# Kernel tuning notes

Hardware: AMD Instinct MI355X
Metric: run time of the kernel (lower is better)

Reference implementation:

```python
import jax, jax.numpy as jnp
import numpy as np

B, S, IK, IV = 16, 2048, 3, 1
D = IK + IV          # input_size = 4
H = 256              # hidden_size
F = 512              # dim_feedforward
L = 2                # num_layers
EPS = 1e-5


def setup_inputs() -> dict:
    key = jax.random.key(0)
    ks = jax.random.split(key, 16)
    n = jax.random.normal
    inp = {
        'KEY': n(ks[0], (B, S, IK), jnp.float32),
        'VALUE': n(ks[1], (B, S, IV), jnp.float32),
        # per-layer kernel-attention projections (stacked on layer axis)
        'Wq': n(ks[2], (L, D, H), jnp.float32) * 0.1,
        'bq': jnp.zeros((L, H), jnp.float32),
        'Wk': n(ks[3], (L, D, H), jnp.float32) * 0.1,
        'bk': jnp.zeros((L, H), jnp.float32),
        'Wv': n(ks[4], (L, D, H), jnp.float32) * 0.1,
        'bv': jnp.zeros((L, H), jnp.float32),
        'Wo': n(ks[5], (L, H, D), jnp.float32) * 0.1,
        'bo': jnp.zeros((L, D), jnp.float32),
        'bw': jnp.ones((L,), jnp.float32),          # Gaussian kernel bandwidth
        # LayerNorm 1
        'g1': jnp.ones((L, D), jnp.float32),
        'be1': jnp.zeros((L, D), jnp.float32),
        # FFN
        'W1': n(ks[6], (L, D, F), jnp.float32) * 0.1,
        'b1': jnp.zeros((L, F), jnp.float32),
        'W2': n(ks[7], (L, F, D), jnp.float32) * 0.1,
        'b2': jnp.zeros((L, D), jnp.float32),
        # LayerNorm 2
        'g2': jnp.ones((L, D), jnp.float32),
        'be2': jnp.zeros((L, D), jnp.float32),
        # final fc: input_size -> input_v
        'Wfc': n(ks[8], (D, IV), jnp.float32) * 0.1,
        'bfc': jnp.zeros((IV,), jnp.float32),
    }
    return inp


def _layernorm(x, g, b):
    m = x.mean(-1, keepdims=True)
    v = ((x - m) ** 2).mean(-1, keepdims=True)
    return (x - m) * jax.lax.rsqrt(v + EPS) * g + b


def reference(KEY, VALUE, Wq, bq, Wk, bk, Wv, bv, Wo, bo, bw,
              g1, be1, W1, b1, W2, b2, g2, be2, Wfc, bfc):
    # positioning: concat coords and values -> [B, S, D]
    X = jnp.concatenate([KEY, VALUE], axis=-1)
    n_layers = Wq.shape[0]
    for i in range(n_layers):
        # Nadaraya-Watson Gaussian kernel attention (madsnn, type='nwd', kernel='gauss')
        Q = X @ Wq[i] + bq[i]                      # [B,S,H]
        K = X @ Wk[i] + bk[i]                      # [B,S,H]
        V = X @ Wv[i] + bv[i]                      # [B,S,H]
        # pairwise squared distances ||q-k||^2, [B,S,S]
        d2 = ((Q * Q).sum(-1)[:, :, None]
              + (K * K).sum(-1)[:, None, :]
              - 2.0 * jnp.einsum('bqh,bkh->bqk', Q, K))
        attn = jax.nn.softmax(-0.5 * d2 * (bw[i] ** 2), axis=-1)
        attn_out = jnp.einsum('bqk,bkh->bqh', attn, V) @ Wo[i] + bo[i]  # [B,S,D]
        # residual + LayerNorm + FFN + residual + LayerNorm (dropout = identity in eval)
        res = _layernorm(X + attn_out, g1[i], be1[i])
        ff = jax.nn.relu(res @ W1[i] + b1[i]) @ W2[i] + b2[i]
        X = _layernorm(res + ff, g2[i], be2[i])
    return X @ Wfc + bfc                            # [B,S,IV]
```

## Files before the change

### kernel.cpp

```cpp
#include <hip/hip_runtime.h>

#define BB 16
#define SS 2048
#define NTOK (BB*SS)
#define NPAIR (NTOK/2)
#define PLANE (NPAIR*4)
#define FF 512
#define EPSF 1e-5f

#if __has_builtin(__builtin_amdgcn_exp2f)
#define EXP2F(x) __builtin_amdgcn_exp2f(x)
#else
#define EXP2F(x) exp2f(x)
#endif

typedef float v2f __attribute__((ext_vector_type(2)));


__device__ __forceinline__ float wred64(float v) {
#pragma unroll
  for (int m = 32; m > 0; m >>= 1) v += __shfl_xor(v, m, 64);
  return v;
}

__device__ __forceinline__ float rflf(float v) {
  union { float f; int i; } u; u.f = v;
  u.i = __builtin_amdgcn_readfirstlane(u.i);
  return u.f;
}


__global__ __launch_bounds__(64) void prep_kernel(
    const float* __restrict__ Wq, const float* __restrict__ bq,
    const float* __restrict__ Wk, const float* __restrict__ bk,
    const float* __restrict__ Wv, const float* __restrict__ bv,
    const float* __restrict__ Wo, const float* __restrict__ bw,
    const float* __restrict__ W1, const float* __restrict__ b1,
    const float* __restrict__ W2,
    float* __restrict__ sm, float* __restrict__ w1t)
{
  const int i = blockIdx.x;
  const int lane = threadIdx.x;
  float m4[4][4] = {{0}}, gkk[4][4] = {{0}}, wvo[4][4] = {{0}};
  float akk[4] = {0}, bvo[4] = {0};
  float ck1 = 0.f, ck2 = 0.f;

  for (int h = lane; h < 256; h += 64) {
    float vq[4], vk[4], vv[4], wo4[4];
#pragma unroll
    for (int a = 0; a < 4; ++a) {
      vq[a]  = Wq[(i*4 + a)*256 + h];
      vk[a]  = Wk[(i*4 + a)*256 + h];
      vv[a]  = Wv[(i*4 + a)*256 + h];
      wo4[a] = Wo[(i*256 + h)*4 + a];
    }
    const float bqh = bq[i*256 + h], bkh = bk[i*256 + h], bvh = bv[i*256 + h];
#pragma unroll
    for (int a = 0; a < 4; ++a) {
#pragma unroll
      for (int c = 0; c < 4; ++c) {
        m4[a][c]  = fmaf(vq[a], vk[c], m4[a][c]);
        gkk[a][c] = fmaf(vk[a], vk[c], gkk[a][c]);
        wvo[a][c] = fmaf(vv[a], wo4[c], wvo[a][c]);
      }
      akk[a] = fmaf(vk[a], bqh - bkh, akk[a]);
      bvo[a] = fmaf(bvh, wo4[a], bvo[a]);
    }
    ck1 = fmaf(bqh, bkh, ck1);
    ck2 = fmaf(bkh, bkh, ck2);
  }
#pragma unroll
  for (int a = 0; a < 4; ++a) {
#pragma unroll
    for (int c = 0; c < 4; ++c) {
      m4[a][c]  = wred64(m4[a][c]);
      gkk[a][c] = wred64(gkk[a][c]);
      wvo[a][c] = wred64(wvo[a][c]);
    }
    akk[a] = wred64(akk[a]);
    bvo[a] = wred64(bvo[a]);
  }
  ck1 = wred64(ck1); ck2 = wred64(ck2);

  if (lane == 0) {
    const float bwv = bw[i];
    const float bw2 = bwv * bwv * 1.44269504088896f;
    float* s = sm + i*64;
#pragma unroll
    for (int a = 0; a < 4; ++a) {
#pragma unroll
      for (int c = 0; c < 4; ++c) {
        s[a*4+c]      = bw2 * m4[a][c];
        s[16 + a*4+c] = -0.5f * bw2 * gkk[a][c];
        s[32 + a*4+c] = wvo[a][c];
      }
      s[48+a] = bw2 * akk[a];
      s[52+a] = bvo[a];
    }
    s[56] = bw2 * (ck1 - 0.5f * ck2);
  }
  for (int f = lane; f < FF; f += 64) {
    float* rec = w1t + (i*FF + f)*12;
#pragma unroll
    for (int c = 0; c < 4; ++c) rec[c]   = W1[(i*4 + c)*FF + f];
#pragma unroll
    for (int c = 0; c < 4; ++c) rec[4+c] = W2[(i*FF + f)*4 + c];
    rec[8] = b1[i*FF + f];
    rec[9] = 0.f; rec[10] = 0.f; rec[11] = 0.f;
  }
}

__device__ __forceinline__ void compute_feat(const float x[4], const float* __restrict__ s,
                                             float* __restrict__ featrec)
{
  float P[4], VT[4], tk[4];
#pragma unroll
  for (int a = 0; a < 4; ++a) {
    P[a]  = fmaf(s[a*4+3], x[3], fmaf(s[a*4+2], x[2], fmaf(s[a*4+1], x[1], s[a*4+0]*x[0])));
    tk[a] = fmaf(s[16+a*4+3], x[3], fmaf(s[16+a*4+2], x[2], fmaf(s[16+a*4+1], x[1], s[16+a*4+0]*x[0])));
    VT[a] = s[52+a] + fmaf(s[32+3*4+a], x[3], fmaf(s[32+2*4+a], x[2], fmaf(s[32+1*4+a], x[1], s[32+0*4+a]*x[0])));
  }
  float R = s[56];
#pragma unroll
  for (int a = 0; a < 4; ++a) R = fmaf(tk[a] + s[48+a], x[a], R);
  featrec[0]=P[0]; featrec[1]=P[1]; featrec[2]=P[2]; featrec[3]=P[3];
  featrec[4]=VT[0]; featrec[5]=VT[1]; featrec[6]=VT[2]; featrec[7]=VT[3];
  featrec[8]=R;
}

__global__ __launch_bounds__(256) void feat_kernel(
    const float* __restrict__ KEY, const float* __restrict__ VALUE,
    const float* __restrict__ sm, float* __restrict__ feat)
{
  const int p = blockIdx.x*256 + threadIdx.x;
  const int ta = 2*p, tb = 2*p + 1;
  float xa[4] = {KEY[ta*3], KEY[ta*3+1], KEY[ta*3+2], VALUE[ta]};
  float xb[4] = {KEY[tb*3], KEY[tb*3+1], KEY[tb*3+2], VALUE[tb]};
  float fa[9], fb[9];
  compute_feat(xa, sm, fa);
  compute_feat(xb, sm, fb);
#pragma unroll
  for (int pl = 0; pl < 4; ++pl) {
    *(float4*)(feat + (size_t)pl*PLANE + (size_t)p*4) =
        make_float4(fa[2*pl], fb[2*pl], fa[2*pl+1], fb[2*pl+1]);
  }
  *(float4*)(feat + (size_t)4*PLANE + (size_t)p*4) =
      make_float4(fa[8], fb[8], 0.f, 0.f);
}

__device__ __forceinline__ void ln4(const float t[4], const float* __restrict__ g,
                                    const float* __restrict__ b, float r[4])
{
  const float m = 0.25f*(t[0]+t[1]+t[2]+t[3]);
  const float d0 = t[0]-m, d1 = t[1]-m, d2 = t[2]-m, d3 = t[3]-m;
  const float v = 0.25f*(d0*d0 + d1*d1 + d2*d2 + d3*d3);
  const float sc = rsqrtf(v + EPSF);
  r[0] = fmaf(d0*sc, g[0], b[0]);
  r[1] = fmaf(d1*sc, g[1], b[1]);
  r[2] = fmaf(d2*sc, g[2], b[2]);
  r[3] = fmaf(d3*sc, g[3], b[3]);
}

__global__ __launch_bounds__(512, 4) void layer_kernel(
    const float* __restrict__ KEY, const float* __restrict__ VALUE,
    const float* __restrict__ X, const float* __restrict__ feat,
    const float* __restrict__ w1t, const float* __restrict__ smn,
    const float* __restrict__ bo, const float* __restrict__ g1, const float* __restrict__ be1,
    const float* __restrict__ b2v, const float* __restrict__ g2, const float* __restrict__ be2,
    float* __restrict__ Xout, float* __restrict__ featout,
    const float* __restrict__ Wfc, const float* __restrict__ bfc,
    float* __restrict__ outp, int first, int last)
{
  const int bid = blockIdx.x;
  const int b = bid >> 5, qg = bid & 31;
  const int qbase = (b << 11) + (qg << 6);
  const int tid = threadIdx.x;
  const int lane = tid & 63, wv = tid >> 6;
  const int q0 = qbase + wv*8;

  __shared__ float sums[8*8*9];
  __shared__ float ress[64*4];
  __shared__ float redf[8*64*4];

  float qx0[8], qx1[8], qx2[8], qx3[8];
#pragma unroll
  for (int q = 0; q < 8; ++q) {
    const int gq = q0 + q;
    float a, bq_, c, d;
    if (first) {
      a = KEY[gq*3]; bq_ = KEY[gq*3+1]; c = KEY[gq*3+2]; d = VALUE[gq];
    } else {
      const float4 xv = *(const float4*)(X + (size_t)gq*4);
      a = xv.x; bq_ = xv.y; c = xv.z; d = xv.w;
    }
    qx0[q] = rflf(a); qx1[q] = rflf(bq_); qx2[q] = rflf(c); qx3[q] = rflf(d);
  }

  v2f aV0[8], aV1[8], aV2[8], aV3[8], aD[8];
#pragma unroll
  for (int q = 0; q < 8; ++q) {
    aV0[q] = v2f{0.f,0.f}; aV1[q] = v2f{0.f,0.f};
    aV2[q] = v2f{0.f,0.f}; aV3[q] = v2f{0.f,0.f};
    aD[q]  = v2f{0.f,0.f};
  }

  const int pb = (b << 10) + lane;
#pragma unroll 2
  for (int it = 0; it < 16; ++it) {
    const size_t p4 = (size_t)(pb + (it << 6)) * 4;
    const float4 A = *(const float4*)(feat + p4);
    const float4 Bf = *(const float4*)(feat + (size_t)PLANE + p4);
    const float4 C = *(const float4*)(feat + (size_t)2*PLANE + p4);
    const float4 D = *(const float4*)(feat + (size_t)3*PLANE + p4);
    const float4 E = *(const float4*)(feat + (size_t)4*PLANE + p4);
    const v2f P0 = v2f{A.x, A.y},  P1 = v2f{A.z, A.w};
    const v2f P2 = v2f{Bf.x, Bf.y}, P3 = v2f{Bf.z, Bf.w};
    const v2f V0 = v2f{C.x, C.y},  V1 = v2f{C.z, C.w};
    const v2f V2 = v2f{D.x, D.y},  V3 = v2f{D.z, D.w};
    const v2f Rp = v2f{E.x, E.y};
#pragma unroll
    for (int q = 0; q < 8; ++q) {
      v2f l = __builtin_elementwise_fma(P0, v2f{qx0[q], qx0[q]}, Rp);
      l = __builtin_elementwise_fma(P1, v2f{qx1[q], qx1[q]}, l);
      l = __builtin_elementwise_fma(P2, v2f{qx2[q], qx2[q]}, l);
      l = __builtin_elementwise_fma(P3, v2f{qx3[q], qx3[q]}, l);
      const v2f e = v2f{EXP2F(l.x), EXP2F(l.y)};
      aV0[q] = __builtin_elementwise_fma(e, V0, aV0[q]);
      aV1[q] = __builtin_elementwise_fma(e, V1, aV1[q]);
      aV2[q] = __builtin_elementwise_fma(e, V2, aV2[q]);
      aV3[q] = __builtin_elementwise_fma(e, V3, aV3[q]);
      aD[q] += e;
    }
  }

  float s[8][5];
#pragma unroll
  for (int q = 0; q < 8; ++q) {
    s[q][0] = aV0[q].x + aV0[q].y;
    s[q][1] = aV1[q].x + aV1[q].y;
    s[q][2] = aV2[q].x + aV2[q].y;
    s[q][3] = aV3[q].x + aV3[q].y;
    s[q][4] = aD[q].x + aD[q].y;
  }
#pragma unroll
  for (int q = 0; q < 8; ++q)
#pragma unroll
    for (int c = 0; c < 5; ++c) s[q][c] = wred64(s[q][c]);

  if (lane == 0) {
    float* dst = sums + wv*72;
#pragma unroll
    for (int q = 0; q < 8; ++q) {
#pragma unroll
      for (int c = 0; c < 5; ++c) dst[q*9 + c] = s[q][c];
    }
  }
  __syncthreads();

  if (tid < 64) {
    const float* sv = sums + tid*9;
    const float inv = 1.0f / sv[4];
    const int gq = qbase + tid;
    float xv0, xv1, xv2, xv3;
    if (first) {
      xv0 = KEY[gq*3]; xv1 = KEY[gq*3+1]; xv2 = KEY[gq*3+2]; xv3 = VALUE[gq];
    } else {
      const float4 xv = *(const float4*)(X + (size_t)gq*4);
      xv0 = xv.x; xv1 = xv.y; xv2 = xv.z; xv3 = xv.w;
    }
    float t4[4];
    t4[0] = xv0 + fmaf(sv[0], inv, bo[0]);
    t4[1] = xv1 + fmaf(sv[1], inv, bo[1]);
    t4[2] = xv2 + fmaf(sv[2], inv, bo[2]);
    t4[3] = xv3 + fmaf(sv[3], inv, bo[3]);
    float r[4];
    ln4(t4, g1, be1, r);
    *(float4*)(ress + tid*4) = make_float4(r[0], r[1], r[2], r[3]);
  }
  __syncthreads();

  const int tok = lane, fc = wv;
  const float4 rv = *(const float4*)(ress + tok*4);
  float fa0 = 0.f, fa1 = 0.f, fa2 = 0.f, fa3 = 0.f;
  const float* wt = w1t + (size_t)fc*64*12;
#pragma unroll 4
  for (int f = 0; f < 64; ++f) {
    const float* rec = wt + f*12;
    const float4 w1r = *(const float4*)rec;
    const float4 w2r = *(const float4*)(rec + 4);
    const float b1f = rec[8];
    float h = fmaf(rv.w, w1r.w, fmaf(rv.z, w1r.z, fmaf(rv.y, w1r.y, fmaf(rv.x, w1r.x, b1f))));
    h = fmaxf(h, 0.f);
    fa0 = fmaf(h, w2r.x, fa0);
    fa1 = fmaf(h, w2r.y, fa1);
    fa2 = fmaf(h, w2r.z, fa2);
    fa3 = fmaf(h, w2r.w, fa3);
  }
  *(float4*)(redf + (size_t)((fc << 6) + tok)*4) = make_float4(fa0, fa1, fa2, fa3);
  __syncthreads();

  if (tid < 64) {
    float t2[4];
#pragma unroll
    for (int c = 0; c < 4; ++c) {
      float sa = b2v[c];
#pragma unroll
      for (int k = 0; k < 8; ++k) sa += redf[(size_t)((k << 6) + tid)*4 + c];
      t2[c] = ress[tid*4 + c] + sa;
    }
    float y[4];
    ln4(t2, g2, be2, y);
    const int gq = qbase + tid;
    if (last) {
      outp[gq] = fmaf(y[3], Wfc[3], fmaf(y[2], Wfc[2], fmaf(y[1], Wfc[1], fmaf(y[0], Wfc[0], bfc[0]))));
    } else {
      *(float4*)(Xout + (size_t)gq*4) = make_float4(y[0], y[1], y[2], y[3]);
      float fr[9];
      compute_feat(y, smn, fr);
      const int p = gq >> 1, par = gq & 1;
#pragma unroll
      for (int c = 0; c < 8; ++c)
        featout[(size_t)(c >> 1)*PLANE + (size_t)p*4 + (c & 1)*2 + par] = fr[c];
      featout[(size_t)4*PLANE + (size_t)p*4 + par] = fr[8];
    }
  }
}

extern "C" void kernel_launch(void* const* d_in, const int* in_sizes, int n_in,
                              void* d_out, int out_size, void* d_ws, size_t ws_size,
                              hipStream_t stream)
{
  const float* KEY   = (const float*)d_in[0];
  const float* VALUE = (const float*)d_in[1];
  const float* Wq  = (const float*)d_in[2];
  const float* bq  = (const float*)d_in[3];
  const float* Wk  = (const float*)d_in[4];
  const float* bk  = (const float*)d_in[5];
  const float* Wv  = (const float*)d_in[6];
  const float* bv  = (const float*)d_in[7];
  const float* Wo  = (const float*)d_in[8];
  const float* bo  = (const float*)d_in[9];
  const float* bw  = (const float*)d_in[10];
  const float* g1  = (const float*)d_in[11];
  const float* be1 = (const float*)d_in[12];
  const float* W1  = (const float*)d_in[13];
  const float* b1  = (const float*)d_in[14];
  const float* W2  = (const float*)d_in[15];
  const float* b2  = (const float*)d_in[16];
  const float* g2  = (const float*)d_in[17];
  const float* be2 = (const float*)d_in[18];
  const float* Wfc = (const float*)d_in[19];
  const float* bfc = (const float*)d_in[20];
  float* out = (float*)d_out;

  float* w    = (float*)d_ws;
  float* sm   = w;
  float* w1t  = w + 128;
  float* X1   = w + 12416;
  float* f0   = w + 143488;
  float* f1   = w + 471168;

  prep_kernel<<<2, 64, 0, stream>>>(Wq, bq, Wk, bk, Wv, bv, Wo, bw,
                                    W1, b1, W2, sm, w1t);
  feat_kernel<<<64, 256, 0, stream>>>(KEY, VALUE, sm, f0);

  layer_kernel<<<512, 512, 0, stream>>>(KEY, VALUE, X1, f0,
      w1t, sm + 64,
      bo, g1, be1, b2, g2, be2,
      X1, f1, Wfc, bfc, out, 1, 0);

  layer_kernel<<<512, 512, 0, stream>>>(KEY, VALUE, X1, f1,
      w1t + FF*12, sm,
      bo + 4, g1 + 4, be1 + 4, b2 + 4, g2 + 4, be2 + 4,
      X1, f1, Wfc, bfc, out, 0, 1);
}
```

Measured before the change: 183.1 us.

## Double query work per wave and software-pipeline feature loads in layer kernel

Result: slower. 189.2 us (+3.4%).

```diff
diff --git a/kernel.cpp b/kernel.cpp
--- a/kernel.cpp
+++ b/kernel.cpp
@@ -7,6 +7,7 @@
 #define PLANE (NPAIR*4)
 #define FF 512
 #define EPSF 1e-5f
+#define QW 16
 
 #if __has_builtin(__builtin_amdgcn_exp2f)
 #define EXP2F(x) __builtin_amdgcn_exp2f(x)
@@ -161,7 +162,7 @@
   r[3] = fmaf(d3*sc, g[3], b[3]);
 }
 
-__global__ __launch_bounds__(512, 4) void layer_kernel(
+__global__ __launch_bounds__(256, 2) void layer_kernel(
     const float* __restrict__ KEY, const float* __restrict__ VALUE,
     const float* __restrict__ X, const float* __restrict__ feat,
     const float* __restrict__ w1t, const float* __restrict__ smn,
@@ -176,50 +177,45 @@
   const int qbase = (b << 11) + (qg << 6);
   const int tid = threadIdx.x;
   const int lane = tid & 63, wv = tid >> 6;
-  const int q0 = qbase + wv*8;
-
-  __shared__ float sums[8*8*9];
+  const int q0 = qbase + wv*QW;
+
+  __shared__ float sums[4*QW*9];
   __shared__ float ress[64*4];
-  __shared__ float redf[8*64*4];
-
-  float qx0[8], qx1[8], qx2[8], qx3[8];
-#pragma unroll
-  for (int q = 0; q < 8; ++q) {
+  __shared__ float redf[4*64*4];
+
+  float qx0[QW], qx1[QW], qx2[QW], qx3[QW];
+#pragma unroll
+  for (int q = 0; q < QW; ++q) {
     const int gq = q0 + q;
-    float a, bq_, c, d;
+    float a, b_, c, d;
     if (first) {
-      a = KEY[gq*3]; bq_ = KEY[gq*3+1]; c = KEY[gq*3+2]; d = VALUE[gq];
+      a = KEY[gq*3]; b_ = KEY[gq*3+1]; c = KEY[gq*3+2]; d = VALUE[gq];
     } else {
       const float4 xv = *(const float4*)(X + (size_t)gq*4);
-      a = xv.x; bq_ = xv.y; c = xv.z; d = xv.w;
-    }
-    qx0[q] = rflf(a); qx1[q] = rflf(bq_); qx2[q] = rflf(c); qx3[q] = rflf(d);
-  }
-
-  v2f aV0[8], aV1[8], aV2[8], aV3[8], aD[8];
-#pragma unroll
-  for (int q = 0; q < 8; ++q) {
+      a = xv.x; b_ = xv.y; c = xv.z; d = xv.w;
+    }
+    qx0[q] = rflf(a); qx1[q] = rflf(b_); qx2[q] = rflf(c); qx3[q] = rflf(d);
+  }
+
+  v2f aV0[QW], aV1[QW], aV2[QW], aV3[QW], aD[QW];
+#pragma unroll
+  for (int q = 0; q < QW; ++q) {
     aV0[q] = v2f{0.f,0.f}; aV1[q] = v2f{0.f,0.f};
     aV2[q] = v2f{0.f,0.f}; aV3[q] = v2f{0.f,0.f};
     aD[q]  = v2f{0.f,0.f};
   }
 
   const int pb = (b << 10) + lane;
-#pragma unroll 2
-  for (int it = 0; it < 16; ++it) {
-    const size_t p4 = (size_t)(pb + (it << 6)) * 4;
-    const float4 A = *(const float4*)(feat + p4);
-    const float4 Bf = *(const float4*)(feat + (size_t)PLANE + p4);
-    const float4 C = *(const float4*)(feat + (size_t)2*PLANE + p4);
-    const float4 D = *(const float4*)(feat + (size_t)3*PLANE + p4);
-    const float4 E = *(const float4*)(feat + (size_t)4*PLANE + p4);
-    const v2f P0 = v2f{A.x, A.y},  P1 = v2f{A.z, A.w};
+
+  auto PROC = [&](const float4& A, const float4& Bf, const float4& C,
+                  const float4& D, const float4& E) {
+    const v2f P0 = v2f{A.x, A.y},   P1 = v2f{A.z, A.w};
     const v2f P2 = v2f{Bf.x, Bf.y}, P3 = v2f{Bf.z, Bf.w};
-    const v2f V0 = v2f{C.x, C.y},  V1 = v2f{C.z, C.w};
-    const v2f V2 = v2f{D.x, D.y},  V3 = v2f{D.z, D.w};
+    const v2f V0 = v2f{C.x, C.y},   V1 = v2f{C.z, C.w};
+    const v2f V2 = v2f{D.x, D.y},   V3 = v2f{D.z, D.w};
     const v2f Rp = v2f{E.x, E.y};
 #pragma unroll
-    for (int q = 0; q < 8; ++q) {
+    for (int q = 0; q < QW; ++q) {
       v2f l = __builtin_elementwise_fma(P0, v2f{qx0[q], qx0[q]}, Rp);
       l = __builtin_elementwise_fma(P1, v2f{qx1[q], qx1[q]}, l);
       l = __builtin_elementwise_fma(P2, v2f{qx2[q], qx2[q]}, l);
@@ -231,11 +227,31 @@
       aV3[q] = __builtin_elementwise_fma(e, V3, aV3[q]);
       aD[q] += e;
     }
-  }
-
-  float s[8][5];
-#pragma unroll
-  for (int q = 0; q < 8; ++q) {
+  };
+
+#define LDCH(A_, B_, C_, D_, E_, it_) {                                  \
+    const size_t o = (size_t)(pb + ((it_) << 6)) * 4;                    \
+    A_ = *(const float4*)(feat + o);                                     \
+    B_ = *(const float4*)(feat + (size_t)PLANE + o);                     \
+    C_ = *(const float4*)(feat + (size_t)2*PLANE + o);                   \
+    D_ = *(const float4*)(feat + (size_t)3*PLANE + o);                   \
+    E_ = *(const float4*)(feat + (size_t)4*PLANE + o); }
+
+  float4 pA, pB, pC, pD, pE;
+  float4 nA, nB, nC, nD, nE;
+  LDCH(pA, pB, pC, pD, pE, 0);
+#pragma unroll
+  for (int it = 0; it < 16; it += 2) {
+    LDCH(nA, nB, nC, nD, nE, it + 1);
+    PROC(pA, pB, pC, pD, pE);
+    if (it + 2 < 16) LDCH(pA, pB, pC, pD, pE, it + 2);
+    PROC(nA, nB, nC, nD, nE);
+  }
+#undef LDCH
+
+  float s[QW][5];
+#pragma unroll
+  for (int q = 0; q < QW; ++q) {
     s[q][0] = aV0[q].x + aV0[q].y;
     s[q][1] = aV1[q].x + aV1[q].y;
     s[q][2] = aV2[q].x + aV2[q].y;
@@ -243,14 +259,14 @@
     s[q][4] = aD[q].x + aD[q].y;
   }
 #pragma unroll
-  for (int q = 0; q < 8; ++q)
+  for (int q = 0; q < QW; ++q)
 #pragma unroll
     for (int c = 0; c < 5; ++c) s[q][c] = wred64(s[q][c]);
 
   if (lane == 0) {
-    float* dst = sums + wv*72;
-#pragma unroll
-    for (int q = 0; q < 8; ++q) {
+    float* dst = sums + wv*(QW*9);
+#pragma unroll
+    for (int q = 0; q < QW; ++q) {
 #pragma unroll
       for (int c = 0; c < 5; ++c) dst[q*9 + c] = s[q][c];
     }
@@ -282,9 +298,9 @@
   const int tok = lane, fc = wv;
   const float4 rv = *(const float4*)(ress + tok*4);
   float fa0 = 0.f, fa1 = 0.f, fa2 = 0.f, fa3 = 0.f;
-  const float* wt = w1t + (size_t)fc*64*12;
+  const float* wt = w1t + (size_t)fc*128*12;
 #pragma unroll 4
-  for (int f = 0; f < 64; ++f) {
+  for (int f = 0; f < 128; ++f) {
     const float* rec = wt + f*12;
     const float4 w1r = *(const float4*)rec;
     const float4 w2r = *(const float4*)(rec + 4);
@@ -305,7 +321,7 @@
     for (int c = 0; c < 4; ++c) {
       float sa = b2v[c];
 #pragma unroll
-      for (int k = 0; k < 8; ++k) sa += redf[(size_t)((k << 6) + tid)*4 + c];
+      for (int k = 0; k < 4; ++k) sa += redf[(size_t)((k << 6) + tid)*4 + c];
       t2[c] = ress[tid*4 + c] + sa;
     }
     float y[4];
@@ -364,12 +380,12 @@
                                     W1, b1, W2, sm, w1t);
   feat_kernel<<<64, 256, 0, stream>>>(KEY, VALUE, sm, f0);
 
-  layer_kernel<<<512, 512, 0, stream>>>(KEY, VALUE, X1, f0,
+  layer_kernel<<<512, 256, 0, stream>>>(KEY, VALUE, X1, f0,
       w1t, sm + 64,
       bo, g1, be1, b2, g2, be2,
       X1, f1, Wfc, bfc, out, 1, 0);
 
-  layer_kernel<<<512, 512, 0, stream>>>(KEY, VALUE, X1, f1,
+  layer_kernel<<<512, 256, 0, stream>>>(KEY, VALUE, X1, f1,
       w1t + FF*12, sm,
       bo + 4, g1 + 4, be1 + 4, b2 + 4, g2 + 4, be2 + 4,
       X1, f1, Wfc, bfc, out, 0, 1);
```
